# Optimization experiments

Hardware: AMD Instinct MI355X
Metric: run time of the kernel (lower is better)

The kernel has to match this reference:

```python
import jax, jax.numpy as jnp
import numpy as np

KERNEL_MUL = 2.0
KERNEL_NUM = 5
EPS = 1e-3


def setup_inputs() -> dict:
    key = jax.random.key(0)
    k1, k2 = jax.random.split(key)
    source = jax.random.normal(k1, (2048, 512), dtype=jnp.float32)
    target = jax.random.normal(k2, (2048, 512), dtype=jnp.float32)
    beta = jnp.ones((KERNEL_NUM,), dtype=jnp.float32) / KERNEL_NUM
    return {"source": source, "target": target, "beta": beta}


def _sq_dists(total):
    # squared Euclidean pairwise distances, (N, N), clamped >= 0 (matches cdist(p=2)**2)
    sq = jnp.sum(total * total, axis=-1)
    d = sq[:, None] + sq[None, :] - 2.0 * (total @ total.T)
    return jnp.maximum(d, 0.0)


def _project_simplex(v):
    m = v.shape[0]
    mu = -jnp.sort(-v)                      # descending
    cs = jnp.cumsum(mu)
    ar = jnp.arange(1, m + 1, dtype=v.dtype)
    cond = mu - (cs - 1.0) / ar > 0
    idx = jnp.where(cond, jnp.arange(m), -1)
    rho = jnp.where(jnp.any(cond), jnp.max(idx), 0)
    theta = (cs[rho] - 1.0) / (rho + 1).astype(v.dtype)
    p = jnp.maximum(v - theta, 0.0)
    return p / (p.sum() + 1e-12)


def _update_beta(source, target, beta):
    # Batched version of the per-pair quad-kernel loop in _update_beta.
    Ns, D = source.shape
    Nt = target.shape[0]
    P = min(Ns // 2, Nt // 2)  # num_effective_pairs (static)
    s = source[: 2 * P].reshape(P, 2, D)
    t = target[: 2 * P].reshape(P, 2, D)
    quad = jnp.concatenate([s, t], axis=1)              # (P, 4, D) -> [s1, s2, t1, t2]
    diff = quad[:, :, None, :] - quad[:, None, :, :]
    sq = jnp.sum(diff * diff, axis=-1)                  # (P, 4, 4)
    offdiag = ~np.eye(4, dtype=bool)
    bw = jnp.median(sq[:, offdiag], axis=1) + 1e-6      # per-pair median of nonzero dists
    bw = bw / (KERNEL_MUL ** (KERNEL_NUM // 2))
    bws = bw[:, None] * (KERNEL_MUL ** jnp.arange(KERNEL_NUM, dtype=bw.dtype))[None, :]
    K = jnp.exp(-sq[:, None, :, :] / bws[:, :, None, None])   # (P, 5, 4, 4)
    g = K[:, :, 0, 1] + K[:, :, 2, 3] - K[:, :, 0, 2] - K[:, :, 1, 3]  # (P, 5)
    gm = jnp.mean(g, axis=0)
    Q = (g.T @ g) / P - jnp.outer(gm, gm) + EPS * jnp.eye(KERNEL_NUM, dtype=g.dtype)
    # projected gradient descent on the simplex (lr=1, max_iter=100, tol=1e-6)
    def cond_fn(st):
        _, _, i, conv = st
        return (i < 100) & (~conv)
    def body_fn(st):
        b, _, i, _ = st
        proj = _project_simplex(b - Q @ b)
        conv = jnp.linalg.norm(proj - b) < 1e-6
        return (proj, proj, i + 1, conv)
    _, proj, _, _ = jax.lax.while_loop(
        cond_fn, body_fn, (beta, beta, jnp.int32(0), jnp.array(False)))
    return proj


def _forward(source, target, beta):
    beta_new = _update_beta(jax.lax.stop_gradient(source),
                            jax.lax.stop_gradient(target), beta)
    Ns = source.shape[0]
    total = jnp.concatenate([source, target], axis=0)   # (N, D)
    N = total.shape[0]
    sq = _sq_dists(total)                               # (N, N)
    offdiag = ~np.eye(N, dtype=bool)
    bw = jnp.median(sq[offdiag]) + 1e-6
    bw = bw / (KERNEL_MUL ** (KERNEL_NUM // 2))
    bws = bw * (KERNEL_MUL ** jnp.arange(KERNEL_NUM, dtype=sq.dtype))  # (5,)
    Ks = jnp.exp(-sq[None, :, :] / bws[:, None, None])  # (5, N, N)
    joint = jnp.einsum('k,kij->ij', beta_new, Ks)
    XX = joint[:Ns, :Ns]
    YY = joint[Ns:, Ns:]
    XY = joint[:Ns, Ns:]
    n = XX.shape[0]
    m = YY.shape[0]
    term_XX = (jnp.sum(XX) - jnp.trace(XX)) / (n * (n - 1))
    term_YY = (jnp.sum(YY) - jnp.trace(YY)) / (m * (m - 1))
    term_XY = jnp.sum(XY) / (n * m)
    loss = term_XX + term_YY - 2.0 * term_XY
    return jnp.maximum(loss, 0.0)


def reference(source, target, beta):
    return _forward(source, target, beta)
```

## Files before the change

### kernel.cpp

```cpp
#include <hip/hip_runtime.h>
#include <math.h>

#define NT 4096
#define NS 2048
#define DDIM 512
#define KN 5
#define NTILES 528
#define RANKA 8386559u
#define RANKB 8386560u

typedef __bf16 bf16x8 __attribute__((ext_vector_type(8)));
typedef float f32x4 __attribute__((ext_vector_type(4)));
typedef unsigned short u16x8 __attribute__((ext_vector_type(8)));

static __device__ inline unsigned short f2bf(float x) {
    unsigned u = __float_as_uint(x);
    unsigned r = (u + 0x7fffu + ((u >> 16) & 1u)) >> 16;
    return (unsigned short)r;
}
static __device__ inline float bf2f(unsigned short h) {
    return __uint_as_float(((unsigned)h) << 16);
}

static __device__ inline void tri_map(int b, int& bx, int& by) {
    int x = (int)((sqrtf(8.0f * (float)b + 1.0f) - 1.0f) * 0.5f);
    while ((x + 1) * (x + 2) / 2 <= b) ++x;
    while (x * (x + 1) / 2 > b) --x;
    bx = x;
    by = b - x * (x + 1) / 2;
}

static __device__ inline void wscan(const unsigned* __restrict__ h, int C, unsigned r,
                                    unsigned& bin, unsigned& rem)
{
    int lane = threadIdx.x;
    unsigned s = 0;
    for (int i = 0; i < C; ++i) s += h[lane * C + i];
    unsigned x = s;
    #pragma unroll
    for (int off = 1; off < 64; off <<= 1) {
        unsigned y = __shfl_up(x, off);
        if (lane >= off) x += y;
    }
    unsigned base = x - s;
    bool has = (r >= base) && (r < base + s);
    unsigned long long mm = __ballot(has);
    int leader = __ffsll(mm) - 1;
    unsigned b = 0, cb = 0;
    if (lane == leader) {
        unsigned cc = base;
        for (int i = 0; i < C; ++i) {
            unsigned hv = h[lane * C + i];
            if (r < cc + hv) { b = lane * C + i; cb = cc; break; }
            cc += hv;
        }
    }
    bin = __shfl(b, leader);
    rem = r - __shfl(cb, leader);
}

static __device__ void beta_solve(const float* __restrict__ g,
                                  const float* __restrict__ beta_in,
                                  float* __restrict__ beta_out)
{
    int lane = threadIdx.x;
    float gs[KN] = {0, 0, 0, 0, 0};
    float gg[15];
    #pragma unroll
    for (int i = 0; i < 15; ++i) gg[i] = 0.0f;
    for (int p = lane; p < 1024; p += 64) {
        float gv[KN];
        #pragma unroll
        for (int k = 0; k < KN; ++k) gv[k] = g[(size_t)p * KN + k];
        int idx = 0;
        #pragma unroll
        for (int a2 = 0; a2 < KN; ++a2) {
            gs[a2] += gv[a2];
            #pragma unroll
            for (int b2 = a2; b2 < KN; ++b2) gg[idx++] += gv[a2] * gv[b2];
        }
    }
    #pragma unroll
    for (int m = 32; m > 0; m >>= 1) {
        #pragma unroll
        for (int k = 0; k < KN; ++k) gs[k] += __shfl_xor(gs[k], m);
        #pragma unroll
        for (int i = 0; i < 15; ++i) gg[i] += __shfl_xor(gg[i], m);
    }
    if (lane != 0) return;

    float Q[KN][KN], gm[KN];
    #pragma unroll
    for (int k = 0; k < KN; ++k) gm[k] = gs[k] * (1.0f / 1024.0f);
    int idx = 0;
    #pragma unroll
    for (int a2 = 0; a2 < KN; ++a2)
        #pragma unroll
        for (int b2 = a2; b2 < KN; ++b2) {
            float qv = gg[idx++] * (1.0f / 1024.0f) - gm[a2] * gm[b2];
            Q[a2][b2] = qv; Q[b2][a2] = qv;
        }
    #pragma unroll
    for (int k = 0; k < KN; ++k) Q[k][k] += 0.001f;

    float b[KN], proj[KN];
    #pragma unroll
    for (int k = 0; k < KN; ++k) { b[k] = beta_in[k]; proj[k] = b[k]; }
    for (int it = 0; it < 100; ++it) {
        float v[KN];
        #pragma unroll
        for (int a2 = 0; a2 < KN; ++a2) {
            float qb = Q[a2][0] * b[0] + Q[a2][1] * b[1] + Q[a2][2] * b[2]
                     + Q[a2][3] * b[3] + Q[a2][4] * b[4];
            v[a2] = b[a2] - qb;
        }
        float mu0 = v[0], mu1 = v[1], mu2 = v[2], mu3 = v[3], mu4 = v[4];
#define CMPSW(x, y) { float hi_ = fmaxf(x, y); float lo_ = fminf(x, y); x = hi_; y = lo_; }
        CMPSW(mu0, mu1) CMPSW(mu3, mu4) CMPSW(mu2, mu4) CMPSW(mu2, mu3)
        CMPSW(mu0, mu3) CMPSW(mu0, mu2) CMPSW(mu1, mu4) CMPSW(mu1, mu3) CMPSW(mu1, mu2)
#undef CMPSW
        float cs0 = mu0, cs1 = cs0 + mu1, cs2 = cs1 + mu2, cs3 = cs2 + mu3, cs4 = cs3 + mu4;
        bool c1 = mu1 * 2.0f > cs1 - 1.0f;
        bool c2 = mu2 * 3.0f > cs2 - 1.0f;
        bool c3 = mu3 * 4.0f > cs3 - 1.0f;
        bool c4 = mu4 * 5.0f > cs4 - 1.0f;
        float csSel = cs0, rcpSel = 1.0f;
        if (c1) { csSel = cs1; rcpSel = 0.5f; }
        if (c2) { csSel = cs2; rcpSel = (1.0f / 3.0f); }
        if (c3) { csSel = cs3; rcpSel = 0.25f; }
        if (c4) { csSel = cs4; rcpSel = 0.2f; }
        float theta = (csSel - 1.0f) * rcpSel;
        float ssum = 0.0f;
        #pragma unroll
        for (int k = 0; k < KN; ++k) { proj[k] = fmaxf(v[k] - theta, 0.0f); ssum += proj[k]; }
        float invs = 1.0f / (ssum + 1e-12f);
        float nd = 0.0f;
        #pragma unroll
        for (int k = 0; k < KN; ++k) {
            proj[k] *= invs;
            float dd = proj[k] - b[k];
            nd += dd * dd;
            b[k] = proj[k];
        }
        if (nd < 1e-12f) break;
    }
    #pragma unroll
    for (int k = 0; k < KN; ++k) beta_out[k] = proj[k];
}

__global__ __launch_bounds__(256) void k_prep2(const float* __restrict__ S,
                                               const float* __restrict__ T,
                                               unsigned short* __restrict__ Hi,
                                               unsigned short* __restrict__ Lo,
                                               float* __restrict__ norms,
                                               float* __restrict__ g,
                                               unsigned* __restrict__ hists)
{
    if (blockIdx.x < 45) hists[blockIdx.x * 256 + threadIdx.x] = 0;
    int p = blockIdx.x * 4 + (threadIdx.x >> 6);
    int l = threadIdx.x & 63;
    const float* r0 = S + (size_t)(2 * p) * DDIM;
    const float* r1 = r0 + DDIM;
    const float* r2 = T + (size_t)(2 * p) * DDIM;
    const float* r3 = r2 + DDIM;
    float a[8], b[8], c[8], d[8];
    *(float4*)&a[0] = *(const float4*)(r0 + l * 8); *(float4*)&a[4] = *(const float4*)(r0 + l * 8 + 4);
    *(float4*)&b[0] = *(const float4*)(r1 + l * 8); *(float4*)&b[4] = *(const float4*)(r1 + l * 8 + 4);
    *(float4*)&c[0] = *(const float4*)(r2 + l * 8); *(float4*)&c[4] = *(const float4*)(r2 + l * 8 + 4);
    *(float4*)&d[0] = *(const float4*)(r3 + l * 8); *(float4*)&d[4] = *(const float4*)(r3 + l * 8 + 4);

    float n0 = 0, n1 = 0, n2 = 0, n3 = 0;
    float s01 = 0, s23 = 0, s02 = 0, s13 = 0, s03 = 0, s12 = 0;
    u16x8 h0, l0, h1, l1, h2, l2, h3, l3;
    #pragma unroll
    for (int k = 0; k < 8; ++k) {
        float va = a[k], vb = b[k], vc = c[k], vd = d[k];
        n0 += va * va; n1 += vb * vb; n2 += vc * vc; n3 += vd * vd;
        float t01 = va - vb, t23 = vc - vd, t02 = va - vc, t13 = vb - vd;
        s01 += t01*t01; s23 += t23*t23; s02 += t02*t02; s13 += t13*t13;
        float t03 = va - vd, t12 = vb - vc;
        s03 += t03*t03; s12 += t12*t12;
        unsigned short hh;
        hh = f2bf(va); h0[k] = hh; l0[k] = f2bf(va - bf2f(hh));
        hh = f2bf(vb); h1[k] = hh; l1[k] = f2bf(vb - bf2f(hh));
        hh = f2bf(vc); h2[k] = hh; l2[k] = f2bf(vc - bf2f(hh));
        hh = f2bf(vd); h3[k] = hh; l3[k] = f2bf(vd - bf2f(hh));
    }
    size_t g0 = (size_t)(2 * p) * DDIM + l * 8;
    size_t g1 = g0 + DDIM;
    size_t g2 = (size_t)(NS + 2 * p) * DDIM + l * 8;
    size_t g3 = g2 + DDIM;
    *(u16x8*)&Hi[g0] = h0; *(u16x8*)&Lo[g0] = l0;
    *(u16x8*)&Hi[g1] = h1; *(u16x8*)&Lo[g1] = l1;
    *(u16x8*)&Hi[g2] = h2; *(u16x8*)&Lo[g2] = l2;
    *(u16x8*)&Hi[g3] = h3; *(u16x8*)&Lo[g3] = l3;

    #pragma unroll
    for (int m = 32; m > 0; m >>= 1) {
        n0 += __shfl_xor(n0, m); n1 += __shfl_xor(n1, m);
        n2 += __shfl_xor(n2, m); n3 += __shfl_xor(n3, m);
        s01 += __shfl_xor(s01, m); s23 += __shfl_xor(s23, m);
        s02 += __shfl_xor(s02, m); s13 += __shfl_xor(s13, m);
        s03 += __shfl_xor(s03, m); s12 += __shfl_xor(s12, m);
    }
    if (l == 0) {
        norms[2 * p] = n0; norms[2 * p + 1] = n1;
        norms[NS + 2 * p] = n2; norms[NS + 2 * p + 1] = n3;
        float v[6] = { s01, s02, s03, s12, s13, s23 };
        for (int i = 0; i < 5; ++i)
            for (int j = 0; j < 5 - i; ++j)
                if (v[j] > v[j + 1]) { float t = v[j]; v[j] = v[j + 1]; v[j + 1] = t; }
        float med = 0.5f * (v[2] + v[3]);
        float bw = (med + 1e-6f) * 0.25f;
        #pragma unroll
        for (int k = 0; k < KN; ++k) {
            float inv = 1.0f / (bw * (float)(1 << k));
            g[(size_t)p * KN + k] = expf(-s01 * inv) + expf(-s23 * inv)
                                  - expf(-s02 * inv) - expf(-s13 * inv);
        }
    }
}

__global__ __launch_bounds__(256) void k_dist_mfma(const unsigned short* __restrict__ Hi,
                                                   const unsigned short* __restrict__ Lo,
                                                   const float* __restrict__ norms,
                                                   float* __restrict__ D,
                                                   const float* __restrict__ g,
                                                   const float* __restrict__ beta_in,
                                                   float* __restrict__ beta_out,
                                                   unsigned* __restrict__ gH)
{
    __shared__ __align__(16) unsigned short sA[2][2][128][32];
    __shared__ __align__(16) unsigned short sB[2][2][128][32];

    if (blockIdx.x == 0) {
        if (threadIdx.x < 64) beta_solve(g, beta_in, beta_out);
        return;
    }

    int bb = blockIdx.x - 1;
    int swz = (bb & 7) * 66 + (bb >> 3);
    int bx, by;
    tri_map(swz, bx, by);
    const int m0 = by * 128, n0 = bx * 128;

    const int tid = threadIdx.x;
    const int w = tid >> 6, l = tid & 63;
    const int wr = w >> 1, wc = w & 1;

    const int chunk = (l & 3) ^ ((((l >> 2) & 3) + ((l >> 4) & 3)) & 3);
    const size_t gA0 = (size_t)(m0 + w * 16 + (l >> 2)) * DDIM + chunk * 8;
    const size_t gA1 = gA0 + (size_t)64 * DDIM;
    const size_t gB0 = (size_t)(n0 + w * 16 + (l >> 2)) * DDIM + chunk * 8;
    const size_t gB1 = gB0 + (size_t)64 * DDIM;
    const unsigned w1024 = w * 1024;

#define GLD(dst, srcptr, goff)                                                      \
    __builtin_amdgcn_global_load_lds(                                               \
        (const __attribute__((address_space(1))) unsigned*)((srcptr) + (goff)),     \
        (__attribute__((address_space(3))) unsigned*)((char*)(dst) + w1024), 16, 0, 0)
#define STAGE(buf, kk)                                  \
    do {                                                \
        GLD(&sA[buf][0][0][0],  Hi, gA0 + (kk));        \
        GLD(&sA[buf][0][64][0], Hi, gA1 + (kk));        \
        GLD(&sA[buf][1][0][0],  Lo, gA0 + (kk));        \
        GLD(&sA[buf][1][64][0], Lo, gA1 + (kk));        \
        GLD(&sB[buf][0][0][0],  Hi, gB0 + (kk));        \
        GLD(&sB[buf][0][64][0], Hi, gB1 + (kk));        \
        GLD(&sB[buf][1][0][0],  Lo, gB0 + (kk));        \
        GLD(&sB[buf][1][64][0], Lo, gB1 + (kk));        \
    } while (0)

    f32x4 acc[4][4] = {};
    const int q = l >> 4;
    const int fr = ((l & 3) + ((l >> 2) & 3)) & 3;
    const unsigned soff = ((unsigned)(q ^ fr)) << 4;
    const unsigned rowbA = (wr * 64 + (l & 15)) * 64 + soff;
    const unsigned rowbB = (wc * 64 + (l & 15)) * 64 + soff;

    STAGE(0, 0);
    __syncthreads();

    #pragma unroll 2
    for (int t = 0; t < 16; ++t) {
        const int cur = t & 1;
        if (t < 15) STAGE(cur ^ 1, (t + 1) * 32);

        bf16x8 ah[4], al[4], bh[4], bl[4];
        #pragma unroll
        for (int m = 0; m < 4; ++m) {
            ah[m] = *(const bf16x8*)((const char*)&sA[cur][0][0][0] + rowbA + m * 1024);
            al[m] = *(const bf16x8*)((const char*)&sA[cur][1][0][0] + rowbA + m * 1024);
        }
        #pragma unroll
        for (int n = 0; n < 4; ++n) {
            bh[n] = *(const bf16x8*)((const char*)&sB[cur][0][0][0] + rowbB + n * 1024);
            bl[n] = *(const bf16x8*)((const char*)&sB[cur][1][0][0] + rowbB + n * 1024);
        }
        #pragma unroll
        for (int m = 0; m < 4; ++m)
            #pragma unroll
            for (int n = 0; n < 4; ++n) {
                acc[m][n] = __builtin_amdgcn_mfma_f32_16x16x32_bf16(bh[n], ah[m], acc[m][n], 0, 0, 0);
                acc[m][n] = __builtin_amdgcn_mfma_f32_16x16x32_bf16(bl[n], ah[m], acc[m][n], 0, 0, 0);
                acc[m][n] = __builtin_amdgcn_mfma_f32_16x16x32_bf16(bh[n], al[m], acc[m][n], 0, 0, 0);
            }
        __syncthreads();
    }
#undef STAGE
#undef GLD

    float* ncache = (float*)&sB[0][0][0][0];
    unsigned* hrep = (unsigned*)&sB[0][0][0][0] + 256;
    if (tid < 128) ncache[tid] = norms[m0 + tid];
    else           ncache[tid] = norms[n0 + tid - 128];
    for (int i = tid; i < 4096; i += 256) hrep[i] = 0;
    __syncthreads();

    unsigned* hmine = hrep + w * 1024;
    const unsigned wgt = (bx != by) ? 2u : 1u;
    float* rowbuf = (float*)&sA[0][0][0][0] + w * 1024;
    const int rr = l & 15;
    #pragma unroll
    for (int m = 0; m < 4; ++m) {
        float nrm = ncache[wr * 64 + m * 16 + rr];
        #pragma unroll
        for (int n = 0; n < 4; ++n) {
            float4 ncv = *(const float4*)&ncache[128 + wc * 64 + n * 16 + (q << 2)];
            f32x4 a = acc[m][n];
            float4 o;
            o.x = fmaxf(nrm + ncv.x - 2.0f * a[0], 0.0f);
            o.y = fmaxf(nrm + ncv.y - 2.0f * a[1], 0.0f);
            o.z = fmaxf(nrm + ncv.z - 2.0f * a[2], 0.0f);
            o.w = fmaxf(nrm + ncv.w - 2.0f * a[3], 0.0f);
            int ch = (n * 4 + q) ^ (rr & 7);
            *(float4*)(rowbuf + rr * 64 + ch * 4) = o;
        }
        #pragma unroll
        for (int s = 0; s < 4; ++s) {
            int row = s * 4 + q;
            int ch = (l & 15) ^ (row & 7);
            float4 v = *(const float4*)(rowbuf + row * 64 + ch * 4);
            int rowg = m0 + wr * 64 + m * 16 + row;
            int colg = n0 + wc * 64 + (l & 15) * 4;
            *(float4*)&D[(size_t)rowg * NT + colg] = v;
            unsigned b0_ = __float_as_uint(v.x) >> 22;
            unsigned b1_ = __float_as_uint(v.y) >> 22;
            unsigned b2_ = __float_as_uint(v.z) >> 22;
            unsigned b3_ = __float_as_uint(v.w) >> 22;
            unsigned pb = b0_, pc = (rowg == colg) ? 0u : wgt;
            unsigned cj;
            cj = (rowg == colg + 1) ? 0u : wgt;
            if (b1_ == pb) pc += cj; else { if (pc) atomicAdd(&hmine[pb], pc); pb = b1_; pc = cj; }
            cj = (rowg == colg + 2) ? 0u : wgt;
            if (b2_ == pb) pc += cj; else { if (pc) atomicAdd(&hmine[pb], pc); pb = b2_; pc = cj; }
            cj = (rowg == colg + 3) ? 0u : wgt;
            if (b3_ == pb) pc += cj; else { if (pc) atomicAdd(&hmine[pb], pc); pb = b3_; pc = cj; }
            if (pc) atomicAdd(&hmine[pb], pc);
        }
    }
    __syncthreads();
    for (int i = tid; i < 1024; i += 256) {
        unsigned c = hrep[i] + hrep[i + 1024] + hrep[i + 2048] + hrep[i + 3072];
        if (c) atomicAdd(&gH[i], c);
    }
}

__global__ __launch_bounds__(256) void k_h1(const float* __restrict__ D,
                                            const unsigned* __restrict__ gH,
                                            unsigned* __restrict__ g1A,
                                            unsigned* __restrict__ g1B)
{
    __shared__ unsigned lha[1024];
    __shared__ unsigned lhb[1024];
    __shared__ unsigned sres[2];
    int tid = threadIdx.x;
    for (int i = tid; i < 1024; i += 256) { lha[i] = 0; lhb[i] = 0; }
    if (tid < 64) {
        unsigned pA, remA, pB, remB;
        wscan(gH, 16, RANKA, pA, remA);
        wscan(gH, 16, RANKB, pB, remB);
        if (tid == 0) { sres[0] = pA; sres[1] = pB; }
    }
    __syncthreads();
    unsigned pA = sres[0], pB = sres[1];
    int bx, by;
    tri_map(blockIdx.x, bx, by);
    int m0 = by * 128, n0 = bx * 128;
    unsigned wt = (bx != by) ? 2u : 1u;
    for (int v = tid; v < 4096; v += 256) {
        int r = m0 + (v >> 5);
        int c0 = n0 + (v & 31) * 4;
        float4 dv = *(const float4*)&D[(size_t)r * NT + c0];
        const float* dd = (const float*)&dv;
        #pragma unroll
        for (int j = 0; j < 4; ++j) {
            if (r == c0 + j) continue;
            unsigned key = __float_as_uint(dd[j]);
            if ((key >> 22) == pA) atomicAdd(&lha[(key >> 12) & 1023], wt);
            if ((key >> 22) == pB) atomicAdd(&lhb[(key >> 12) & 1023], wt);
        }
    }
    __syncthreads();
    for (int i = tid; i < 1024; i += 256) {
        unsigned ca = lha[i];
        if (ca) atomicAdd(&g1A[i], ca);
        unsigned cb = lhb[i];
        if (cb) atomicAdd(&g1B[i], cb);
    }
}

__global__ __launch_bounds__(256) void k_h2(const float* __restrict__ D,
                                            const unsigned* __restrict__ gH,
                                            const unsigned* __restrict__ g1A,
                                            const unsigned* __restrict__ g1B,
                                            unsigned* __restrict__ g2A,
                                            unsigned* __restrict__ g2B)
{
    __shared__ unsigned lha[4096];
    __shared__ unsigned lhb[4096];
    __shared__ unsigned sres[2];
    int tid = threadIdx.x;
    for (int i = tid; i < 4096; i += 256) { lha[i] = 0; lhb[i] = 0; }
    if (tid < 64) {
        unsigned pA, remA, pB, remB, b1A, r1A, b1B, r1B;
        wscan(gH, 16, RANKA, pA, remA);
        wscan(gH, 16, RANKB, pB, remB);
        wscan(g1A, 16, remA, b1A, r1A);
        wscan(g1B, 16, remB, b1B, r1B);
        if (tid == 0) { sres[0] = (pA << 10) | b1A; sres[1] = (pB << 10) | b1B; }
    }
    __syncthreads();
    unsigned preA = sres[0], preB = sres[1];
    int bx, by;
    tri_map(blockIdx.x, bx, by);
    int m0 = by * 128, n0 = bx * 128;
    unsigned wt = (bx != by) ? 2u : 1u;
    for (int v = tid; v < 4096; v += 256) {
        int r = m0 + (v >> 5);
        int c0 = n0 + (v & 31) * 4;
        float4 dv = *(const float4*)&D[(size_t)r * NT + c0];
        const float* dd = (const float*)&dv;
        #pragma unroll
        for (int j = 0; j < 4; ++j) {
            if (r == c0 + j) continue;
            unsigned key = __float_as_uint(dd[j]);
            if ((key >> 12) == preA) atomicAdd(&lha[key & 4095], wt);
            if ((key >> 12) == preB) atomicAdd(&lhb[key & 4095], wt);
        }
    }
    __syncthreads();
    for (int i = tid; i < 4096; i += 256) {
        unsigned ca = lha[i];
        if (ca) atomicAdd(&g2A[i], ca);
        unsigned cb = lhb[i];
        if (cb) atomicAdd(&g2B[i], cb);
    }
}

__global__ __launch_bounds__(256) void k_wsumf(const float* __restrict__ D,
                                               const unsigned* __restrict__ gH,
                                               const unsigned* __restrict__ g1A,
                                               const unsigned* __restrict__ g1B,
                                               const unsigned* __restrict__ g2A,
                                               const unsigned* __restrict__ g2B,
                                               const float* __restrict__ beta,
                                               double* __restrict__ partials,
                                               unsigned* __restrict__ cnt,
                                               float* __restrict__ out)
{
    __shared__ double red[256];
    __shared__ unsigned sres[2];
    __shared__ unsigned tk;
    int tid = threadIdx.x;
    if (tid < 64) {
        unsigned pA, remA, pB, remB, b1A, r1A, b1B, r1B, b2A, r2A, b2B, r2B;
        wscan(gH, 16, RANKA, pA, remA);
        wscan(gH, 16, RANKB, pB, remB);
        wscan(g1A, 16, remA, b1A, r1A);
        wscan(g1B, 16, remB, b1B, r1B);
        wscan(g2A, 64, r1A, b2A, r2A);
        wscan(g2B, 64, r1B, b2B, r2B);
        if (tid == 0) {
            sres[0] = (((pA << 10) | b1A) << 12) | b2A;
            sres[1] = (((pB << 10) | b1B) << 12) | b2B;
        }
    }
    __syncthreads();
    float med = 0.5f * (__uint_as_float(sres[0]) + __uint_as_float(sres[1]));
    float bw = (med + 1e-6f) * 0.25f;
    float i0 = 1.0f / (bw * 1.0f);
    float i1 = 1.0f / (bw * 2.0f);
    float i2 = 1.0f / (bw * 4.0f);
    float i3 = 1.0f / (bw * 8.0f);
    float i4 = 1.0f / (bw * 16.0f);
    float b0 = beta[0], b1 = beta[1], b2 = beta[2], b3 = beta[3], b4 = beta[4];
    const double wDiag = 1.0 / ((double)NS * (NS - 1));
    const double wOff = -1.0 / ((double)NS * NS);
    int bx, by;
    tri_map(blockIdx.x, bx, by);
    int m0 = by * 128, n0 = bx * 128;
    double wt = (bx != by) ? 2.0 : 1.0;
    double acc = 0.0;
    for (int v = tid; v < 4096; v += 256) {
        int r = m0 + (v >> 5);
        int c0 = n0 + (v & 31) * 4;
        float4 dv = *(const float4*)&D[(size_t)r * NT + c0];
        const float* dd = (const float*)&dv;
        #pragma unroll
        for (int j = 0; j < 4; ++j) {
            int c = c0 + j;
            if (r == c) continue;
            float sq = dd[j];
            float val = b0 * __expf(-sq * i0) + b1 * __expf(-sq * i1) + b2 * __expf(-sq * i2)
                      + b3 * __expf(-sq * i3) + b4 * __expf(-sq * i4);
            bool same = (r < NS) == (c < NS);
            acc += (same ? wDiag : wOff) * (double)val;
        }
    }
    acc *= wt;
    red[tid] = acc;
    __syncthreads();
    for (int off = 128; off > 0; off >>= 1) {
        if (tid < off) red[tid] += red[tid + off];
        __syncthreads();
    }
    if (tid == 0) {
        partials[blockIdx.x] = red[0];
        __threadfence();
        tk = atomicAdd(&cnt[0], 1u);
    }
    __syncthreads();
    if (tk == NTILES - 1) {
        __threadfence();
        double a2 = 0.0;
        for (int i = tid; i < NTILES; i += 256) {
            unsigned long long u = atomicAdd((unsigned long long*)&partials[i], 0ull);
            a2 += __longlong_as_double(u);
        }
        red[tid] = a2;
        __syncthreads();
        for (int off = 128; off > 0; off >>= 1) {
            if (tid < off) red[tid] += red[tid + off];
            __syncthreads();
        }
        if (tid == 0) out[0] = (float)fmax(red[0], 0.0);
    }
}

extern "C" void kernel_launch(void* const* d_in, const int* in_sizes, int n_in,
                              void* d_out, int out_size, void* d_ws, size_t ws_size,
                              hipStream_t stream)
{
    const float* S = (const float*)d_in[0];
    const float* T = (const float*)d_in[1];
    const float* beta = (const float*)d_in[2];
    float* out = (float*)d_out;

    float* D = (float*)d_ws;
    unsigned short* Hi = (unsigned short*)(D + (size_t)NT * NT);
    unsigned short* Lo = Hi + (size_t)NT * DDIM;
    float* norms = (float*)(Lo + (size_t)NT * DDIM);
    float* g = norms + NT;
    float* beta2 = g + 1024 * KN;
    unsigned* hists = (unsigned*)(beta2 + 8);
    unsigned* hL0 = hists;
    unsigned* g1A = hists + 1024;
    unsigned* g1B = hists + 2048;
    unsigned* g2A = hists + 3072;
    unsigned* g2B = hists + 7168;
    unsigned* cnt = hists + 11264;
    double* partials = (double*)(hists + 11520);

    k_prep2<<<dim3(256), dim3(256), 0, stream>>>(S, T, Hi, Lo, norms, g, hists);
    k_dist_mfma<<<dim3(NTILES + 1), dim3(256), 0, stream>>>(Hi, Lo, norms, D, g, beta, beta2, hL0);
    k_h1<<<dim3(NTILES), dim3(256), 0, stream>>>(D, hL0, g1A, g1B);
    k_h2<<<dim3(NTILES), dim3(256), 0, stream>>>(D, hL0, g1A, g1B, g2A, g2B);
    k_wsumf<<<dim3(NTILES), dim3(256), 0, stream>>>(D, hL0, g1A, g1B, g2A, g2B,
                                                    beta2, partials, cnt, out);
}
```

Measured before the change: 156.6 us.

## Restructure median radix select and replace five exps with one exp plus squarings

Reworks the exact-median radix selection: the first-level histogram is widened to 12 bits, a bf16-truncated copy of the distance matrix is written for a cheap 4-bit refinement pass, and small single-wave scan kernels compute selection prefixes once instead of every block rescanning. The loss kernel now computes only the widest-bandwidth exponential and obtains the other four by repeated squaring, since the bandwidths are powers of two. This adds an extra full pass over D, an extra write of a 16-bit matrix, and more kernel launches. It also changes rounding in the kernel sum slightly.

```diff
diff --git a/kernel.cpp b/kernel.cpp
--- a/kernel.cpp
+++ b/kernel.cpp
@@ -28,6 +28,10 @@
     while (x * (x + 1) / 2 > b) --x;
     bx = x;
     by = b - x * (x + 1) / 2;
+}
+
+static __device__ inline int xcd_tile(int bb) {
+    return (bb & 7) * 66 + (bb >> 3);
 }
 
 static __device__ inline void wscan(const unsigned* __restrict__ h, int C, unsigned r,
@@ -57,6 +61,26 @@
     }
     bin = __shfl(b, leader);
     rem = r - __shfl(cb, leader);
+}
+
+static __device__ inline unsigned scan16(const unsigned* __restrict__ h, unsigned r, unsigned& rem)
+{
+    int lane = threadIdx.x;
+    unsigned c = (lane < 16) ? h[lane] : 0u;
+    unsigned x = c;
+    #pragma unroll
+    for (int off = 1; off < 16; off <<= 1) {
+        unsigned y = __shfl_up(x, off);
+        if (lane >= off) x += y;
+    }
+    unsigned base = x - c;
+    bool has = (lane < 16) && (r >= base) && (r < base + c);
+    unsigned long long mm = __ballot(has);
+    int leader = __ffsll(mm) - 1;
+    unsigned bin = __shfl((unsigned)lane, leader);
+    unsigned cb = __shfl(base, leader);
+    rem = r - cb;
+    return bin;
 }
 
 static __device__ void beta_solve(const float* __restrict__ g,
@@ -154,9 +178,14 @@
                                                unsigned short* __restrict__ Lo,
                                                float* __restrict__ norms,
                                                float* __restrict__ g,
-                                               unsigned* __restrict__ hists)
-{
-    if (blockIdx.x < 45) hists[blockIdx.x * 256 + threadIdx.x] = 0;
+                                               unsigned* __restrict__ hists,
+                                               unsigned* __restrict__ sel)
+{
+    if (blockIdx.x < 49) hists[blockIdx.x * 256 + threadIdx.x] = 0;
+    if (blockIdx.x == 60 && threadIdx.x == 0) {
+        sel[0] = 0u; sel[1] = RANKA;
+        sel[2] = 0u; sel[3] = RANKB;
+    }
     int p = blockIdx.x * 4 + (threadIdx.x >> 6);
     int l = threadIdx.x & 63;
     const float* r0 = S + (size_t)(2 * p) * DDIM;
@@ -225,6 +254,7 @@
                                                    const unsigned short* __restrict__ Lo,
                                                    const float* __restrict__ norms,
                                                    float* __restrict__ D,
+                                                   unsigned short* __restrict__ D16,
                                                    const float* __restrict__ g,
                                                    const float* __restrict__ beta_in,
                                                    float* __restrict__ beta_out,
@@ -238,10 +268,8 @@
         return;
     }
 
-    int bb = blockIdx.x - 1;
-    int swz = (bb & 7) * 66 + (bb >> 3);
     int bx, by;
-    tri_map(swz, bx, by);
+    tri_map(xcd_tile(blockIdx.x - 1), bx, by);
     const int m0 = by * 128, n0 = bx * 128;
 
     const int tid = threadIdx.x;
@@ -310,16 +338,16 @@
 #undef STAGE
 #undef GLD
 
-    float* ncache = (float*)&sB[0][0][0][0];
-    unsigned* hrep = (unsigned*)&sB[0][0][0][0] + 256;
+    unsigned* hrep = (unsigned*)&sB[0][0][0][0];
+    for (int i = tid; i < 8192; i += 256) hrep[i] = 0;
+    float* ncache = (float*)&sA[0][0][0][0];
     if (tid < 128) ncache[tid] = norms[m0 + tid];
     else           ncache[tid] = norms[n0 + tid - 128];
-    for (int i = tid; i < 4096; i += 256) hrep[i] = 0;
-    __syncthreads();
-
-    unsigned* hmine = hrep + w * 1024;
+    __syncthreads();
+
+    unsigned* hmine = hrep + (w & 1) * 4096;
+    float* rowbuf = (float*)&sA[0][0][0][0] + 256 + w * 1024;
     const unsigned wgt = (bx != by) ? 2u : 1u;
-    float* rowbuf = (float*)&sA[0][0][0][0] + w * 1024;
     const int rr = l & 15;
     #pragma unroll
     for (int m = 0; m < 4; ++m) {
@@ -343,11 +371,18 @@
             float4 v = *(const float4*)(rowbuf + row * 64 + ch * 4);
             int rowg = m0 + wr * 64 + m * 16 + row;
             int colg = n0 + wc * 64 + (l & 15) * 4;
-            *(float4*)&D[(size_t)rowg * NT + colg] = v;
-            unsigned b0_ = __float_as_uint(v.x) >> 22;
-            unsigned b1_ = __float_as_uint(v.y) >> 22;
-            unsigned b2_ = __float_as_uint(v.z) >> 22;
-            unsigned b3_ = __float_as_uint(v.w) >> 22;
+            size_t base = (size_t)rowg * NT + colg;
+            *(float4*)&D[base] = v;
+            ushort4 u;
+            u.x = (unsigned short)(__float_as_uint(v.x) >> 16);
+            u.y = (unsigned short)(__float_as_uint(v.y) >> 16);
+            u.z = (unsigned short)(__float_as_uint(v.z) >> 16);
+            u.w = (unsigned short)(__float_as_uint(v.w) >> 16);
+            *(ushort4*)&D16[base] = u;
+            unsigned b0_ = __float_as_uint(v.x) >> 20;
+            unsigned b1_ = __float_as_uint(v.y) >> 20;
+            unsigned b2_ = __float_as_uint(v.z) >> 20;
+            unsigned b3_ = __float_as_uint(v.w) >> 20;
             unsigned pb = b0_, pc = (rowg == colg) ? 0u : wgt;
             unsigned cj;
             cj = (rowg == colg + 1) ? 0u : wgt;
@@ -360,32 +395,89 @@
         }
     }
     __syncthreads();
-    for (int i = tid; i < 1024; i += 256) {
-        unsigned c = hrep[i] + hrep[i + 1024] + hrep[i + 2048] + hrep[i + 3072];
+    for (int i = tid; i < 4096; i += 256) {
+        unsigned c = hrep[i] + hrep[i + 4096];
         if (c) atomicAdd(&gH[i], c);
     }
 }
 
-__global__ __launch_bounds__(256) void k_h1(const float* __restrict__ D,
-                                            const unsigned* __restrict__ gH,
+__global__ __launch_bounds__(64) void k_s0(const unsigned* __restrict__ gH,
+                                           unsigned* __restrict__ sel)
+{
+    unsigned bA, rA, bB, rB;
+    wscan(gH, 64, sel[1], bA, rA);
+    wscan(gH, 64, sel[3], bB, rB);
+    if (threadIdx.x == 0) {
+        sel[0] = bA; sel[1] = rA;
+        sel[2] = bB; sel[3] = rB;
+    }
+}
+
+__global__ __launch_bounds__(256) void k_h1(const unsigned short* __restrict__ D16,
+                                            const unsigned* __restrict__ sel,
                                             unsigned* __restrict__ g1A,
                                             unsigned* __restrict__ g1B)
 {
-    __shared__ unsigned lha[1024];
-    __shared__ unsigned lhb[1024];
-    __shared__ unsigned sres[2];
+    if (blockIdx.x == 0) return;
+    __shared__ unsigned ha[16], hb[16];
+    if (threadIdx.x < 16) { ha[threadIdx.x] = 0; hb[threadIdx.x] = 0; }
+    unsigned pA = sel[0], pB = sel[2];
+    int bx, by;
+    tri_map(xcd_tile(blockIdx.x - 1), bx, by);
+    int m0 = by * 128, n0 = bx * 128;
+    unsigned wt = (bx != by) ? 2u : 1u;
+    __syncthreads();
+    for (int v = threadIdx.x; v < 2048; v += 256) {
+        int r = m0 + (v >> 4);
+        int c0 = n0 + (v & 15) * 8;
+        u16x8 dv = *(const u16x8*)&D16[(size_t)r * NT + c0];
+        #pragma unroll
+        for (int j = 0; j < 8; ++j) {
+            if (r == c0 + j) continue;
+            unsigned k16 = dv[j];
+            if ((k16 >> 4) == pA) atomicAdd(&ha[k16 & 15], wt);
+            if ((k16 >> 4) == pB) atomicAdd(&hb[k16 & 15], wt);
+        }
+    }
+    __syncthreads();
+    if (threadIdx.x < 16) {
+        unsigned ca = ha[threadIdx.x];
+        if (ca) atomicAdd(&g1A[threadIdx.x], ca);
+        unsigned cb = hb[threadIdx.x];
+        if (cb) atomicAdd(&g1B[threadIdx.x], cb);
+    }
+}
+
+__global__ __launch_bounds__(256) void k_h2a(const float* __restrict__ D,
+                                             const unsigned* __restrict__ sel,
+                                             const unsigned* __restrict__ g1A,
+                                             const unsigned* __restrict__ g1B,
+                                             unsigned* __restrict__ sel4,
+                                             unsigned* __restrict__ g2A,
+                                             unsigned* __restrict__ g2B)
+{
+    __shared__ unsigned lha[4096];
+    __shared__ unsigned lhb[4096];
+    __shared__ unsigned bc[4];
     int tid = threadIdx.x;
-    for (int i = tid; i < 1024; i += 256) { lha[i] = 0; lhb[i] = 0; }
+    for (int i = tid; i < 4096; i += 256) { lha[i] = 0; lhb[i] = 0; }
     if (tid < 64) {
-        unsigned pA, remA, pB, remB;
-        wscan(gH, 16, RANKA, pA, remA);
-        wscan(gH, 16, RANKB, pB, remB);
-        if (tid == 0) { sres[0] = pA; sres[1] = pB; }
-    }
-    __syncthreads();
-    unsigned pA = sres[0], pB = sres[1];
+        unsigned remA, remB;
+        unsigned b1A = scan16(g1A, sel[1], remA);
+        unsigned b1B = scan16(g1B, sel[3], remB);
+        if (tid == 0) {
+            bc[0] = (sel[0] << 4) | b1A; bc[1] = remA;
+            bc[2] = (sel[2] << 4) | b1B; bc[3] = remB;
+        }
+    }
+    __syncthreads();
+    if (blockIdx.x == 0) {
+        if (tid == 0) { sel4[0] = bc[0]; sel4[1] = bc[1]; sel4[2] = bc[2]; sel4[3] = bc[3]; }
+        return;
+    }
+    unsigned preA = bc[0], preB = bc[2];
     int bx, by;
-    tri_map(blockIdx.x, bx, by);
+    tri_map(xcd_tile(blockIdx.x - 1), bx, by);
     int m0 = by * 128, n0 = bx * 128;
     unsigned wt = (bx != by) ? 2u : 1u;
     for (int v = tid; v < 4096; v += 256) {
@@ -397,56 +489,8 @@
         for (int j = 0; j < 4; ++j) {
             if (r == c0 + j) continue;
             unsigned key = __float_as_uint(dd[j]);
-            if ((key >> 22) == pA) atomicAdd(&lha[(key >> 12) & 1023], wt);
-            if ((key >> 22) == pB) atomicAdd(&lhb[(key >> 12) & 1023], wt);
-        }
-    }
-    __syncthreads();
-    for (int i = tid; i < 1024; i += 256) {
-        unsigned ca = lha[i];
-        if (ca) atomicAdd(&g1A[i], ca);
-        unsigned cb = lhb[i];
-        if (cb) atomicAdd(&g1B[i], cb);
-    }
-}
-
-__global__ __launch_bounds__(256) void k_h2(const float* __restrict__ D,
-                                            const unsigned* __restrict__ gH,
-                                            const unsigned* __restrict__ g1A,
-                                            const unsigned* __restrict__ g1B,
-                                            unsigned* __restrict__ g2A,
-                                            unsigned* __restrict__ g2B)
-{
-    __shared__ unsigned lha[4096];
-    __shared__ unsigned lhb[4096];
-    __shared__ unsigned sres[2];
-    int tid = threadIdx.x;
-    for (int i = tid; i < 4096; i += 256) { lha[i] = 0; lhb[i] = 0; }
-    if (tid < 64) {
-        unsigned pA, remA, pB, remB, b1A, r1A, b1B, r1B;
-        wscan(gH, 16, RANKA, pA, remA);
-        wscan(gH, 16, RANKB, pB, remB);
-        wscan(g1A, 16, remA, b1A, r1A);
-        wscan(g1B, 16, remB, b1B, r1B);
-        if (tid == 0) { sres[0] = (pA << 10) | b1A; sres[1] = (pB << 10) | b1B; }
-    }
-    __syncthreads();
-    unsigned preA = sres[0], preB = sres[1];
-    int bx, by;
-    tri_map(blockIdx.x, bx, by);
-    int m0 = by * 128, n0 = bx * 128;
-    unsigned wt = (bx != by) ? 2u : 1u;
-    for (int v = tid; v < 4096; v += 256) {
-        int r = m0 + (v >> 5);
-        int c0 = n0 + (v & 31) * 4;
-        float4 dv = *(const float4*)&D[(size_t)r * NT + c0];
-        const float* dd = (const float*)&dv;
-        #pragma unroll
-        for (int j = 0; j < 4; ++j) {
-            if (r == c0 + j) continue;
-            unsigned key = __float_as_uint(dd[j]);
-            if ((key >> 12) == preA) atomicAdd(&lha[key & 4095], wt);
-            if ((key >> 12) == preB) atomicAdd(&lhb[key & 4095], wt);
+            if ((key >> 16) == preA) atomicAdd(&lha[(key >> 4) & 4095], wt);
+            if ((key >> 16) == preB) atomicAdd(&lhb[(key >> 4) & 4095], wt);
         }
     }
     __syncthreads();
@@ -458,47 +502,89 @@
     }
 }
 
+__global__ __launch_bounds__(64) void k_s2a(const unsigned* __restrict__ sel4,
+                                            const unsigned* __restrict__ g2A,
+                                            const unsigned* __restrict__ g2B,
+                                            unsigned* __restrict__ sel8)
+{
+    unsigned b2A, r2A, b2B, r2B;
+    wscan(g2A, 64, sel4[1], b2A, r2A);
+    wscan(g2B, 64, sel4[3], b2B, r2B);
+    if (threadIdx.x == 0) {
+        sel8[0] = (sel4[0] << 12) | b2A; sel8[1] = r2A;
+        sel8[2] = (sel4[2] << 12) | b2B; sel8[3] = r2B;
+    }
+}
+
+__global__ __launch_bounds__(256) void k_h2b(const float* __restrict__ D,
+                                             const unsigned* __restrict__ sel8,
+                                             unsigned* __restrict__ g3A,
+                                             unsigned* __restrict__ g3B)
+{
+    if (blockIdx.x == 0) return;
+    __shared__ unsigned ha[16], hb[16];
+    if (threadIdx.x < 16) { ha[threadIdx.x] = 0; hb[threadIdx.x] = 0; }
+    unsigned pA = sel8[0], pB = sel8[2];
+    int bx, by;
+    tri_map(xcd_tile(blockIdx.x - 1), bx, by);
+    int m0 = by * 128, n0 = bx * 128;
+    unsigned wt = (bx != by) ? 2u : 1u;
+    __syncthreads();
+    for (int v = threadIdx.x; v < 4096; v += 256) {
+        int r = m0 + (v >> 5);
+        int c0 = n0 + (v & 31) * 4;
+        float4 dv = *(const float4*)&D[(size_t)r * NT + c0];
+        const float* dd = (const float*)&dv;
+        #pragma unroll
+        for (int j = 0; j < 4; ++j) {
+            if (r == c0 + j) continue;
+            unsigned key = __float_as_uint(dd[j]);
+            if ((key >> 4) == pA) atomicAdd(&ha[key & 15], wt);
+            if ((key >> 4) == pB) atomicAdd(&hb[key & 15], wt);
+        }
+    }
+    __syncthreads();
+    if (threadIdx.x < 16) {
+        unsigned ca = ha[threadIdx.x];
+        if (ca) atomicAdd(&g3A[threadIdx.x], ca);
+        unsigned cb = hb[threadIdx.x];
+        if (cb) atomicAdd(&g3B[threadIdx.x], cb);
+    }
+}
+
 __global__ __launch_bounds__(256) void k_wsumf(const float* __restrict__ D,
-                                               const unsigned* __restrict__ gH,
-                                               const unsigned* __restrict__ g1A,
-                                               const unsigned* __restrict__ g1B,
-                                               const unsigned* __restrict__ g2A,
-                                               const unsigned* __restrict__ g2B,
+                                               const unsigned* __restrict__ sel8,
+                                               const unsigned* __restrict__ g3A,
+                                               const unsigned* __restrict__ g3B,
                                                const float* __restrict__ beta,
                                                double* __restrict__ partials,
                                                unsigned* __restrict__ cnt,
                                                float* __restrict__ out)
 {
+    if (blockIdx.x == 0) return;
     __shared__ double red[256];
-    __shared__ unsigned sres[2];
+    __shared__ float sI4;
     __shared__ unsigned tk;
     int tid = threadIdx.x;
     if (tid < 64) {
-        unsigned pA, remA, pB, remB, b1A, r1A, b1B, r1B, b2A, r2A, b2B, r2B;
-        wscan(gH, 16, RANKA, pA, remA);
-        wscan(gH, 16, RANKB, pB, remB);
-        wscan(g1A, 16, remA, b1A, r1A);
-        wscan(g1B, 16, remB, b1B, r1B);
-        wscan(g2A, 64, r1A, b2A, r2A);
-        wscan(g2B, 64, r1B, b2B, r2B);
+        unsigned rA, rB;
+        unsigned b3A = scan16(g3A, sel8[1], rA);
+        unsigned b3B = scan16(g3B, sel8[3], rB);
         if (tid == 0) {
-            sres[0] = (((pA << 10) | b1A) << 12) | b2A;
-            sres[1] = (((pB << 10) | b1B) << 12) | b2B;
-        }
-    }
-    __syncthreads();
-    float med = 0.5f * (__uint_as_float(sres[0]) + __uint_as_float(sres[1]));
-    float bw = (med + 1e-6f) * 0.25f;
-    float i0 = 1.0f / (bw * 1.0f);
-    float i1 = 1.0f / (bw * 2.0f);
-    float i2 = 1.0f / (bw * 4.0f);
-    float i3 = 1.0f / (bw * 8.0f);
-    float i4 = 1.0f / (bw * 16.0f);
+            unsigned keyA = (sel8[0] << 4) | b3A;
+            unsigned keyB = (sel8[2] << 4) | b3B;
+            float med = 0.5f * (__uint_as_float(keyA) + __uint_as_float(keyB));
+            float bw = (med + 1e-6f) * 0.25f;
+            sI4 = 1.0f / (bw * 16.0f);
+        }
+    }
+    __syncthreads();
+    float i4 = sI4;
     float b0 = beta[0], b1 = beta[1], b2 = beta[2], b3 = beta[3], b4 = beta[4];
     const double wDiag = 1.0 / ((double)NS * (NS - 1));
     const double wOff = -1.0 / ((double)NS * NS);
     int bx, by;
-    tri_map(blockIdx.x, bx, by);
+    tri_map(xcd_tile(blockIdx.x - 1), bx, by);
     int m0 = by * 128, n0 = bx * 128;
     double wt = (bx != by) ? 2.0 : 1.0;
     double acc = 0.0;
@@ -512,8 +598,12 @@
             int c = c0 + j;
             if (r == c) continue;
             float sq = dd[j];
-            float val = b0 * __expf(-sq * i0) + b1 * __expf(-sq * i1) + b2 * __expf(-sq * i2)
-                      + b3 * __expf(-sq * i3) + b4 * __expf(-sq * i4);
+            float y1 = __expf(-sq * i4);
+            float y2 = y1 * y1;
+            float y4 = y2 * y2;
+            float y8 = y4 * y4;
+            float y16 = y8 * y8;
+            float val = b4 * y1 + b3 * y2 + b2 * y4 + b1 * y8 + b0 * y16;
             bool same = (r < NS) == (c < NS);
             acc += (same ? wDiag : wOff) * (double)val;
         }
@@ -526,7 +616,7 @@
         __syncthreads();
     }
     if (tid == 0) {
-        partials[blockIdx.x] = red[0];
+        partials[blockIdx.x - 1] = red[0];
         __threadfence();
         tk = atomicAdd(&cnt[0], 1u);
     }
@@ -563,19 +653,30 @@
     float* norms = (float*)(Lo + (size_t)NT * DDIM);
     float* g = norms + NT;
     float* beta2 = g + 1024 * KN;
-    unsigned* hists = (unsigned*)(beta2 + 8);
-    unsigned* hL0 = hists;
-    unsigned* g1A = hists + 1024;
-    unsigned* g1B = hists + 2048;
-    unsigned* g2A = hists + 3072;
-    unsigned* g2B = hists + 7168;
-    unsigned* cnt = hists + 11264;
-    double* partials = (double*)(hists + 11520);
-
-    k_prep2<<<dim3(256), dim3(256), 0, stream>>>(S, T, Hi, Lo, norms, g, hists);
-    k_dist_mfma<<<dim3(NTILES + 1), dim3(256), 0, stream>>>(Hi, Lo, norms, D, g, beta, beta2, hL0);
-    k_h1<<<dim3(NTILES), dim3(256), 0, stream>>>(D, hL0, g1A, g1B);
-    k_h2<<<dim3(NTILES), dim3(256), 0, stream>>>(D, hL0, g1A, g1B, g2A, g2B);
-    k_wsumf<<<dim3(NTILES), dim3(256), 0, stream>>>(D, hL0, g1A, g1B, g2A, g2B,
-                                                    beta2, partials, cnt, out);
-}
+    unsigned* sel = (unsigned*)(beta2 + 8);
+    unsigned* hists = sel + 16;
+    unsigned* gH  = hists;
+    unsigned* g2A = hists + 4096;
+    unsigned* g2B = hists + 8192;
+    unsigned* g1A = hists + 12288;
+    unsigned* g1B = hists + 12304;
+    unsigned* g3A = hists + 12320;
+    unsigned* g3B = hists + 12336;
+    unsigned* cnt = hists + 12352;
+    double* partials = (double*)(hists + 12544);
+    unsigned short* D16 = (unsigned short*)(partials + NTILES);
+
+    unsigned* sel4 = sel + 4;
+    unsigned* sel8 = sel + 8;
+
+    k_prep2<<<dim3(256), dim3(256), 0, stream>>>(S, T, Hi, Lo, norms, g, hists, sel);
+    k_dist_mfma<<<dim3(NTILES + 1), dim3(256), 0, stream>>>(Hi, Lo, norms, D, D16,
+                                                            g, beta, beta2, gH);
+    k_s0<<<dim3(1), dim3(64), 0, stream>>>(gH, sel);
+    k_h1<<<dim3(NTILES + 1), dim3(256), 0, stream>>>(D16, sel, g1A, g1B);
+    k_h2a<<<dim3(NTILES + 1), dim3(256), 0, stream>>>(D, sel, g1A, g1B, sel4, g2A, g2B);
+    k_s2a<<<dim3(1), dim3(64), 0, stream>>>(sel4, g2A, g2B, sel8);
+    k_h2b<<<dim3(NTILES + 1), dim3(256), 0, stream>>>(D, sel8, g3A, g3B);
+    k_wsumf<<<dim3(NTILES + 1), dim3(256), 0, stream>>>(D, sel8, g3A, g3B,
+                                                        beta2, partials, cnt, out);
+}
```

Result: slower. 170.8 us (+9.1%).
